# Optimization experiments

Hardware: AMD Instinct MI355X
Metric: run time of the kernel (lower is better)

## Reference

```python
import jax, jax.numpy as jnp
import numpy as np

N = 16384      # tokens (batch 4 * seq 4096)
H = 4096       # hidden_dim
E = 64         # num_experts
P = 6          # pca_dim = log2(num_experts)
K = 8          # top_k


def setup_inputs() -> dict:
    key = jax.random.key(0)
    k1, k2, k3 = jax.random.split(key, 3)
    return {
        "x": jax.random.normal(k1, (N, H), jnp.float32),
        "pca_mean": jax.random.normal(k2, (H,), jnp.float32) * 0.02,
        "pca_components": jax.random.normal(k3, (P, H), jnp.float32) / np.sqrt(H).astype(np.float32),
        "leaf_centroids": jax.random.normal(jax.random.fold_in(key, 7), (E, P), jnp.float32),
        "top_k": K,
    }


def reference(x, pca_mean, pca_components, leaf_centroids, top_k):
    # PCA projection: (x - mean) @ components.T -> [N, P]
    proj = (x - pca_mean) @ pca_components.T
    # Euclidean cdist to centroids [E, P] via the |a|^2 - 2ab + |b|^2 expansion
    d2 = (jnp.sum(proj * proj, axis=-1, keepdims=True)
          - 2.0 * proj @ leaf_centroids.T
          + jnp.sum(leaf_centroids * leaf_centroids, axis=-1))
    dists = jnp.sqrt(jnp.maximum(d2, 0.0))            # [N, E]
    probs = jax.nn.softmax(-dists, axis=-1)           # [N, E]
    topk_probs, topk_indices = jax.lax.top_k(probs, top_k)
    topk_probs = topk_probs / jnp.sum(topk_probs, axis=-1, keepdims=True)
    return topk_indices, topk_probs, probs
```

## Files before the change

### kernel.cpp

```cpp
#include <hip/hip_runtime.h>

#define N_TOK 16384
#define H_DIM 4096
#define H4    1024
#define P_DIM 6
#define E_NUM 64
#define K_TOP 8
#define BLOCK 256
#define GRID  512
#define TOK_PER_BLOCK 32
#define TOK_PER_WAVE  8
#define TW 4

__launch_bounds__(BLOCK, 1)
__global__ void kdtree_router_kernel(const float* __restrict__ x,
                                     const float* __restrict__ pca_mean,
                                     const float* __restrict__ pca_comp,
                                     const float* __restrict__ centroids,
                                     float* __restrict__ out) {
    __shared__ float4 sW4[P_DIM * H4];
    __shared__ float  sC[P_DIM * E_NUM];
    __shared__ float  sRed[4 * P_DIM];

    const int tid  = threadIdx.x;
    const int wave = tid >> 6;
    const int lane = tid & 63;

    const float4* Wg4   = (const float4*)pca_comp;
    const float4* mean4 = (const float4*)pca_mean;
    const float4* x4    = (const float4*)x;

    for (int i = tid; i < E_NUM * P_DIM; i += BLOCK) {
        int e = i / P_DIM, p = i - e * P_DIM;
        sC[p * E_NUM + e] = centroids[i];
    }

    #pragma unroll
    for (int p = 0; p < P_DIM; ++p) {
        float sp = 0.f;
        for (int i = tid; i < H4; i += BLOCK) {
            float4 w = Wg4[p * H4 + i];
            sW4[p * H4 + i] = w;
            float4 m = mean4[i];
            sp += w.x * m.x + w.y * m.y + w.z * m.z + w.w * m.w;
        }
        #pragma unroll
        for (int off = 32; off > 0; off >>= 1) sp += __shfl_xor(sp, off, 64);
        if (lane == 0) sRed[wave * P_DIM + p] = sp;
    }
    __syncthreads();

    float mp[P_DIM];
    #pragma unroll
    for (int p = 0; p < P_DIM; ++p)
        mp[p] = sRed[p] + sRed[P_DIM + p] + sRed[2 * P_DIM + p] + sRed[3 * P_DIM + p];

    float* out_idx = out;
    float* out_tp  = out + N_TOK * K_TOP;
    float* out_pr  = out + 2 * N_TOK * K_TOP;

    const int tok0 = blockIdx.x * TOK_PER_BLOCK + wave * TOK_PER_WAVE;

    for (int g = 0; g < TOK_PER_WAVE / TW; ++g) {
        const int n0 = tok0 + g * TW;

        float acc[TW][P_DIM];
        #pragma unroll
        for (int t = 0; t < TW; ++t)
            #pragma unroll
            for (int p = 0; p < P_DIM; ++p) acc[t][p] = 0.f;

        float4 xc[TW];
        #pragma unroll
        for (int t = 0; t < TW; ++t) xc[t] = x4[(n0 + t) * H4 + lane];

        for (int it = 0; it < H4 / 64; ++it) {
            float4 xn[TW];
            if (it < H4 / 64 - 1) {
                int h4n = (it + 1) * 64 + lane;
                #pragma unroll
                for (int t = 0; t < TW; ++t) xn[t] = x4[(n0 + t) * H4 + h4n];
            }
            const int h4 = it * 64 + lane;
            float4 w[P_DIM];
            #pragma unroll
            for (int p = 0; p < P_DIM; ++p) w[p] = sW4[p * H4 + h4];

            #pragma unroll
            for (int t = 0; t < TW; ++t) {
                #pragma unroll
                for (int p = 0; p < P_DIM; ++p) {
                    acc[t][p] += xc[t].x * w[p].x + xc[t].y * w[p].y
                               + xc[t].z * w[p].z + xc[t].w * w[p].w;
                }
            }
            if (it < H4 / 64 - 1) {
                #pragma unroll
                for (int t = 0; t < TW; ++t) xc[t] = xn[t];
            }
        }

        #pragma unroll
        for (int t = 0; t < TW; ++t) {
            const int n = n0 + t;
            float pr[P_DIM];
            #pragma unroll
            for (int p = 0; p < P_DIM; ++p) {
                float v = acc[t][p];
                #pragma unroll
                for (int off = 32; off > 0; off >>= 1) v += __shfl_xor(v, off, 64);
                pr[p] = v - mp[p];
            }

            float d2 = 0.f;
            #pragma unroll
            for (int p = 0; p < P_DIM; ++p) {
                float diff = pr[p] - sC[p * E_NUM + lane];
                d2 += diff * diff;
            }
            float dist = sqrtf(d2);

            float mn = dist;
            #pragma unroll
            for (int off = 32; off > 0; off >>= 1) mn = fminf(mn, __shfl_xor(mn, off, 64));
            float ev  = __expf(mn - dist);
            float sum = ev;
            #pragma unroll
            for (int off = 32; off > 0; off >>= 1) sum += __shfl_xor(sum, off, 64);
            float prob = ev / sum;
            out_pr[n * E_NUM + lane] = prob;

            float v = prob; int idx = lane;
            float tsum = 0.f, myv = 0.f; int myi = 0;
            #pragma unroll
            for (int r = 0; r < K_TOP; ++r) {
                float bv = v; int bi = idx;
                #pragma unroll
                for (int off = 32; off > 0; off >>= 1) {
                    float ov = __shfl_xor(bv, off, 64);
                    int   oi = __shfl_xor(bi, off, 64);
                    if (ov > bv || (ov == bv && oi < bi)) { bv = ov; bi = oi; }
                }
                tsum += bv;
                if (lane == r) { myv = bv; myi = bi; }
                if (idx == bi) v = -1.f;
            }
            if (lane < K_TOP) {
                out_idx[n * K_TOP + lane] = (float)myi;
                out_tp [n * K_TOP + lane] = myv / tsum;
            }
        }
    }
}

extern "C" void kernel_launch(void* const* d_in, const int* in_sizes, int n_in,
                              void* d_out, int out_size, void* d_ws, size_t ws_size,
                              hipStream_t stream) {
    const float* x         = (const float*)d_in[0];
    const float* pca_mean  = (const float*)d_in[1];
    const float* pca_comp  = (const float*)d_in[2];
    const float* centroids = (const float*)d_in[3];
    float* out = (float*)d_out;

    kdtree_router_kernel<<<GRID, BLOCK, 0, stream>>>(x, pca_mean, pca_comp, centroids, out);
}
```

Baseline: 454.3 us.

## Use 1024-thread blocks with one token group per wave

Blocks grow from 4 to 16 waves and the grid shrinks from 512 to 256 blocks, with 64 tokens per block. Each wave now handles a single group of 4 tokens, so the outer group loop is gone. More waves per CU are meant to hide the latency of streaming x from global memory. The fixed setup cost of loading the 96 KB PCA weights into shared memory and reducing the mean is now paid once per 64 tokens instead of once per 32.

```diff
diff --git a/kernel.cpp b/kernel.cpp
--- a/kernel.cpp
+++ b/kernel.cpp
@@ -6,13 +6,13 @@
 #define P_DIM 6
 #define E_NUM 64
 #define K_TOP 8
-#define BLOCK 256
-#define GRID  512
-#define TOK_PER_BLOCK 32
-#define TOK_PER_WAVE  8
+#define BLOCK 1024
+#define WAVES 16
+#define GRID  256
+#define TOK_PER_BLOCK 64
 #define TW 4
 
-__launch_bounds__(BLOCK, 1)
+__launch_bounds__(BLOCK, 4)
 __global__ void kdtree_router_kernel(const float* __restrict__ x,
                                      const float* __restrict__ pca_mean,
                                      const float* __restrict__ pca_comp,
@@ -20,7 +20,7 @@
                                      float* __restrict__ out) {
     __shared__ float4 sW4[P_DIM * H4];
     __shared__ float  sC[P_DIM * E_NUM];
-    __shared__ float  sRed[4 * P_DIM];
+    __shared__ float  sRed[WAVES * P_DIM];
 
     const int tid  = threadIdx.x;
     const int wave = tid >> 6;
@@ -30,20 +30,17 @@
     const float4* mean4 = (const float4*)pca_mean;
     const float4* x4    = (const float4*)x;
 
-    for (int i = tid; i < E_NUM * P_DIM; i += BLOCK) {
-        int e = i / P_DIM, p = i - e * P_DIM;
-        sC[p * E_NUM + e] = centroids[i];
+    if (tid < E_NUM * P_DIM) {
+        int e = tid / P_DIM, p = tid - e * P_DIM;
+        sC[p * E_NUM + e] = centroids[tid];
     }
 
     #pragma unroll
     for (int p = 0; p < P_DIM; ++p) {
-        float sp = 0.f;
-        for (int i = tid; i < H4; i += BLOCK) {
-            float4 w = Wg4[p * H4 + i];
-            sW4[p * H4 + i] = w;
-            float4 m = mean4[i];
-            sp += w.x * m.x + w.y * m.y + w.z * m.z + w.w * m.w;
-        }
+        float4 w = Wg4[p * H4 + tid];
+        sW4[p * H4 + tid] = w;
+        float4 m = mean4[tid];
+        float sp = w.x * m.x + w.y * m.y + w.z * m.z + w.w * m.w;
         #pragma unroll
         for (int off = 32; off > 0; off >>= 1) sp += __shfl_xor(sp, off, 64);
         if (lane == 0) sRed[wave * P_DIM + p] = sp;
@@ -52,103 +49,103 @@
 
     float mp[P_DIM];
     #pragma unroll
-    for (int p = 0; p < P_DIM; ++p)
-        mp[p] = sRed[p] + sRed[P_DIM + p] + sRed[2 * P_DIM + p] + sRed[3 * P_DIM + p];
+    for (int p = 0; p < P_DIM; ++p) {
+        float s = 0.f;
+        #pragma unroll
+        for (int w = 0; w < WAVES; ++w) s += sRed[w * P_DIM + p];
+        mp[p] = s;
+    }
 
     float* out_idx = out;
     float* out_tp  = out + N_TOK * K_TOP;
     float* out_pr  = out + 2 * N_TOK * K_TOP;
 
-    const int tok0 = blockIdx.x * TOK_PER_BLOCK + wave * TOK_PER_WAVE;
+    const int n0 = blockIdx.x * TOK_PER_BLOCK + wave * TW;
 
-    for (int g = 0; g < TOK_PER_WAVE / TW; ++g) {
-        const int n0 = tok0 + g * TW;
+    float acc[TW][P_DIM];
+    #pragma unroll
+    for (int t = 0; t < TW; ++t)
+        #pragma unroll
+        for (int p = 0; p < P_DIM; ++p) acc[t][p] = 0.f;
 
-        float acc[TW][P_DIM];
+    float4 xc[TW];
+    #pragma unroll
+    for (int t = 0; t < TW; ++t) xc[t] = x4[(n0 + t) * H4 + lane];
+
+    for (int it = 0; it < H4 / 64; ++it) {
+        float4 xn[TW];
+        if (it < H4 / 64 - 1) {
+            int h4n = (it + 1) * 64 + lane;
+            #pragma unroll
+            for (int t = 0; t < TW; ++t) xn[t] = x4[(n0 + t) * H4 + h4n];
+        }
+        const int h4 = it * 64 + lane;
+        float4 w[P_DIM];
         #pragma unroll
-        for (int t = 0; t < TW; ++t)
-            #pragma unroll
-            for (int p = 0; p < P_DIM; ++p) acc[t][p] = 0.f;
-
-        float4 xc[TW];
-        #pragma unroll
-        for (int t = 0; t < TW; ++t) xc[t] = x4[(n0 + t) * H4 + lane];
-
-        for (int it = 0; it < H4 / 64; ++it) {
-            float4 xn[TW];
-            if (it < H4 / 64 - 1) {
-                int h4n = (it + 1) * 64 + lane;
-                #pragma unroll
-                for (int t = 0; t < TW; ++t) xn[t] = x4[(n0 + t) * H4 + h4n];
-            }
-            const int h4 = it * 64 + lane;
-            float4 w[P_DIM];
-            #pragma unroll
-            for (int p = 0; p < P_DIM; ++p) w[p] = sW4[p * H4 + h4];
-
-            #pragma unroll
-            for (int t = 0; t < TW; ++t) {
-                #pragma unroll
-                for (int p = 0; p < P_DIM; ++p) {
-                    acc[t][p] += xc[t].x * w[p].x + xc[t].y * w[p].y
-                               + xc[t].z * w[p].z + xc[t].w * w[p].w;
-                }
-            }
-            if (it < H4 / 64 - 1) {
-                #pragma unroll
-                for (int t = 0; t < TW; ++t) xc[t] = xn[t];
-            }
-        }
+        for (int p = 0; p < P_DIM; ++p) w[p] = sW4[p * H4 + h4];
 
         #pragma unroll
         for (int t = 0; t < TW; ++t) {
-            const int n = n0 + t;
-            float pr[P_DIM];
             #pragma unroll
             for (int p = 0; p < P_DIM; ++p) {
-                float v = acc[t][p];
-                #pragma unroll
-                for (int off = 32; off > 0; off >>= 1) v += __shfl_xor(v, off, 64);
-                pr[p] = v - mp[p];
+                acc[t][p] += xc[t].x * w[p].x + xc[t].y * w[p].y
+                           + xc[t].z * w[p].z + xc[t].w * w[p].w;
             }
+        }
+        if (it < H4 / 64 - 1) {
+            #pragma unroll
+            for (int t = 0; t < TW; ++t) xc[t] = xn[t];
+        }
+    }
 
-            float d2 = 0.f;
+    #pragma unroll
+    for (int t = 0; t < TW; ++t) {
+        const int n = n0 + t;
+        float pr[P_DIM];
+        #pragma unroll
+        for (int p = 0; p < P_DIM; ++p) {
+            float v = acc[t][p];
             #pragma unroll
-            for (int p = 0; p < P_DIM; ++p) {
-                float diff = pr[p] - sC[p * E_NUM + lane];
-                d2 += diff * diff;
+            for (int off = 32; off > 0; off >>= 1) v += __shfl_xor(v, off, 64);
+            pr[p] = v - mp[p];
+        }
+
+        float d2 = 0.f;
+        #pragma unroll
+        for (int p = 0; p < P_DIM; ++p) {
+            float diff = pr[p] - sC[p * E_NUM + lane];
+            d2 += diff * diff;
+        }
+        float dist = sqrtf(d2);
+
+        float mn = dist;
+        #pragma unroll
+        for (int off = 32; off > 0; off >>= 1) mn = fminf(mn, __shfl_xor(mn, off, 64));
+        float ev  = __expf(mn - dist);
+        float sum = ev;
+        #pragma unroll
+        for (int off = 32; off > 0; off >>= 1) sum += __shfl_xor(sum, off, 64);
+        float prob = ev / sum;
+        out_pr[n * E_NUM + lane] = prob;
+
+        float v = prob; int idx = lane;
+        float tsum = 0.f, myv = 0.f; int myi = 0;
+        #pragma unroll
+        for (int r = 0; r < K_TOP; ++r) {
+            float bv = v; int bi = idx;
+            #pragma unroll
+            for (int off = 32; off > 0; off >>= 1) {
+                float ov = __shfl_xor(bv, off, 64);
+                int   oi = __shfl_xor(bi, off, 64);
+                if (ov > bv || (ov == bv && oi < bi)) { bv = ov; bi = oi; }
             }
-            float dist = sqrtf(d2);
-
-            float mn = dist;
-            #pragma unroll
-            for (int off = 32; off > 0; off >>= 1) mn = fminf(mn, __shfl_xor(mn, off, 64));
-            float ev  = __expf(mn - dist);
-            float sum = ev;
-            #pragma unroll
-            for (int off = 32; off > 0; off >>= 1) sum += __shfl_xor(sum, off, 64);
-            float prob = ev / sum;
-            out_pr[n * E_NUM + lane] = prob;
-
-            float v = prob; int idx = lane;
-            float tsum = 0.f, myv = 0.f; int myi = 0;
-            #pragma unroll
-            for (int r = 0; r < K_TOP; ++r) {
-                float bv = v; int bi = idx;
-                #pragma unroll
-                for (int off = 32; off > 0; off >>= 1) {
-                    float ov = __shfl_xor(bv, off, 64);
-                    int   oi = __shfl_xor(bi, off, 64);
-                    if (ov > bv || (ov == bv && oi < bi)) { bv = ov; bi = oi; }
-                }
-                tsum += bv;
-                if (lane == r) { myv = bv; myi = bi; }
-                if (idx == bi) v = -1.f;
-            }
-            if (lane < K_TOP) {
-                out_idx[n * K_TOP + lane] = (float)myi;
-                out_tp [n * K_TOP + lane] = myv / tsum;
-            }
+            tsum += bv;
+            if (lane == r) { myv = bv; myi = bi; }
+            if (idx == bi) v = -1.f;
+        }
+        if (lane < K_TOP) {
+            out_idx[n * K_TOP + lane] = (float)myi;
+            out_tp [n * K_TOP + lane] = myv / tsum;
         }
     }
 }
```

New measurement: 415.0 us. 8.6% less time.
